# Optimization experiments

Hardware: AMD Instinct MI355X
Metric: run time of the kernel (lower is better)

Reference implementation:

```python
import jax, jax.numpy as jnp
import numpy as np

N = 256    # number of target crystals
FB = 256   # backbone output features
D = 64     # embedding_dim
H = 4      # num_heads
DH = 128   # head_dim
L = 4      # layers
BD = 128   # expansion_size == bias_dim
AK = 100   # amd_k (edge feature dim)
EPS = 1e-5


def mish(x):
    return x * jnp.tanh(jax.nn.softplus(x))


def layernorm(x, g, b):
    m = x.mean(-1, keepdims=True)
    v = x.var(-1, keepdims=True)
    return (x - m) / jnp.sqrt(v + EPS) * g + b


def setup_inputs() -> dict:
    key = jax.random.key(0)
    ks = jax.random.split(key, 16)

    def xavier(k, shape):
        fan_in, fan_out = shape[-2], shape[-1]
        lim = float(np.sqrt(6.0 / (fan_in + fan_out)))
        return jax.random.uniform(k, shape, jnp.float32, -lim, lim)

    return dict(
        target_node_features=jax.random.normal(ks[0], (N, FB), jnp.float32),
        target_edge_features=jax.random.uniform(ks[1], (N, AK), jnp.float32),
        neighbor_target=jax.random.normal(ks[2], (N, 1), jnp.float32),
        embW=xavier(ks[3], (FB, D)), embB=jnp.zeros((D,), jnp.float32),
        boutW=xavier(ks[4], (FB, 1)), boutB=jnp.zeros((1,), jnp.float32),
        qpW=xavier(ks[5], (L, D, H * DH)), qpB=jnp.zeros((L, H * DH), jnp.float32),
        kpW=xavier(ks[6], (L, D, H * DH)), kpB=jnp.zeros((L, H * DH), jnp.float32),
        qoW=xavier(ks[7], (L, H * DH, D)), qoB=jnp.zeros((L, D), jnp.float32),
        koW=xavier(ks[8], (L, H * DH, D)), koB=jnp.zeros((L, D), jnp.float32),
        bpW=xavier(ks[9], (L, BD, H * BD)), bpB=jnp.zeros((L, H * BD), jnp.float32),
        bowW=xavier(ks[10], (L, H * BD, BD)), bowB=jnp.zeros((L, BD), jnp.float32),
        qlnG=jnp.ones((L, D), jnp.float32), qlnB=jnp.zeros((L, D), jnp.float32),
        klnG=jnp.ones((L, D), jnp.float32), klnB=jnp.zeros((L, D), jnp.float32),
    )


def reference(target_node_features, target_edge_features, neighbor_target,
              embW, embB, boutW, boutB, qpW, qpB, kpW, kpB, qoW, qoB,
              koW, koB, bpW, bpB, bowW, bowB, qlnG, qlnB, klnG, klnB):
    n = target_node_features.shape[0]
    dt = target_node_features.dtype
    eye = jnp.eye(n, dtype=dt)
    # neighbors=None path: mask = [1 - I | I], shape [N, 2N]
    mask = jnp.concatenate([1.0 - eye, eye], axis=1)

    predictions = target_node_features @ boutW + boutB          # [N,1]
    node = target_node_features @ embW + embB                   # [N,D]
    q = node
    k = jnp.concatenate([node, node], axis=0)                   # [2N,D]
    edge = jnp.concatenate([target_edge_features, target_edge_features], axis=0)  # [2N,AK]

    # cdist(target_edge, edge) with safe sqrt (zero on the exact-duplicate pairs)
    diff = target_edge_features[:, None, :] - edge[None, :, :]
    sq = jnp.sum(diff * diff, axis=-1)                           # [N,2N]
    d = jnp.where(sq > 0, jnp.sqrt(jnp.where(sq > 0, sq, 1.0)), 0.0)

    # RBFExpansion(vmin=0, vmax=cutoff=1, bins=BD): gamma = 1/mean(diff(centers))
    centers = jnp.linspace(0.0, 1.0, BD).astype(dt)
    gamma = jnp.asarray(BD - 1, dt)
    bias = jnp.exp(-gamma * (d[..., None] - centers) ** 2)       # [N,2N,BD]

    v = jnp.concatenate([neighbor_target, predictions], axis=0)  # [2N,1]

    for l in range(L):
        pq = (q @ qpW[l] + qpB[l]).reshape(n, H, DH)             # [N,H,DH]
        pk = (k @ kpW[l] + kpB[l]).reshape(2 * n, H, DH)         # [2N,H,DH]
        b = jnp.einsum('nmb,bo->nmo', bias, bpW[l]) + bpB[l]     # [N,2N,H*BD]
        diffs = jnp.linalg.norm(b.reshape(n, 2 * n, H, BD), axis=-1)  # [N,2N,H]
        logits = jnp.einsum('nhd,mhd->hnm', pq, pk) / jnp.sqrt(jnp.asarray(DH, dt))
        logits = logits + diffs.transpose(2, 0, 1)               # [H,N,2N]
        logits = jnp.where(mask[None] == 0, -9e15, logits)
        attn = jax.nn.softmax(logits, axis=-1)
        vals = jnp.einsum('hnm,mo->hno', attn, v)                # [H,N,1]
        predictions = jnp.mean(vals[:, :, 0].T, axis=-1, keepdims=True)  # [N,1]
        # permute(1,2,0).reshape: layout is (head_dim, head) interleave
        pq_flat = pq.transpose(0, 2, 1).reshape(n, H * DH)
        pk_flat = pk.transpose(0, 2, 1).reshape(2 * n, H * DH)
        q = layernorm(q + mish(pq_flat @ qoW[l] + qoB[l]), qlnG[l], qlnB[l])
        k = layernorm(k + mish(pk_flat @ koW[l] + koB[l]), klnG[l], klnB[l])
        bias = mish(jnp.einsum('nmb,bo->nmo', b, bowW[l]) + bowB[l])   # [N,2N,BD]
        v = jnp.concatenate([neighbor_target, predictions], axis=0)

    return predictions
```

## Files before the change

kernel.cpp:

```cpp
#include <hip/hip_runtime.h>

struct Params {
  const float *X, *E, *nbr;
  const float *embW, *embB, *boutW, *boutB;
  const float *qpW, *qpB, *kpW, *kpB, *qoW, *qoB, *koW, *koB;
  const float *bpW, *bpB, *bowW, *bowB;
  const float *qlnG, *qlnB, *klnG, *klnB;
  float *out;
  float *pkT;
  float *clsDiff;
  unsigned *bar;
};

__device__ __forceinline__ float mishf(float x) {
  float sp = (x > 20.f) ? x : log1pf(expf(x));
  return x * tanhf(sp);
}

__device__ __forceinline__ void fma4(float4& acc, float s, const float4& v) {
  acc.x = fmaf(s, v.x, acc.x);
  acc.y = fmaf(s, v.y, acc.y);
  acc.z = fmaf(s, v.z, acc.z);
  acc.w = fmaf(s, v.w, acc.w);
}

#define LOAD8(Wp_, J0_, STRIDE_) \
  const float4 w0 = (Wp_)[(size_t)((J0_) + 0) * (STRIDE_)]; \
  const float4 w1 = (Wp_)[(size_t)((J0_) + 1) * (STRIDE_)]; \
  const float4 w2 = (Wp_)[(size_t)((J0_) + 2) * (STRIDE_)]; \
  const float4 w3 = (Wp_)[(size_t)((J0_) + 3) * (STRIDE_)]; \
  const float4 w4 = (Wp_)[(size_t)((J0_) + 4) * (STRIDE_)]; \
  const float4 w5 = (Wp_)[(size_t)((J0_) + 5) * (STRIDE_)]; \
  const float4 w6 = (Wp_)[(size_t)((J0_) + 6) * (STRIDE_)]; \
  const float4 w7 = (Wp_)[(size_t)((J0_) + 7) * (STRIDE_)];

__device__ __forceinline__ void gridBarrier(unsigned* bar, unsigned nblocks) {
  __syncthreads();
  if (threadIdx.x == 0) {
    __threadfence();
    unsigned old = atomicAdd(bar, 1u);
    if (old == nblocks - 1u) {
      atomicExch(bar + 16, 1u);
    } else {
      while (atomicAdd(bar + 16, 0u) == 0u) {
        __builtin_amdgcn_s_sleep(2);
      }
    }
    __threadfence();
  }
  __syncthreads();
}

__device__ void rare_pipe(float* row, float* drow,
                          const float* __restrict__ Wp, const float* __restrict__ Bp,
                          const float* __restrict__ Wo, const float* __restrict__ Bo,
                          float* smW, float* smS, int t) {
  const int lane = t & 63, wave = t >> 6;
  __syncthreads();
  { const int o = t & 511, kh = t >> 9;
    const float* Wc = Wp + (kh * 64) * 512 + o;
    const float* rc = row + kh * 64;
    float a = (kh == 0) ? Bp[o] : 0.f;
    #pragma unroll 8
    for (int c = 0; c < 64; ++c) a = fmaf(rc[c], Wc[c * 512], a);
    smW[t] = a; }
  __syncthreads();
  if (t < 512) smS[t] = smW[t] + smW[512 + t];
  __syncthreads();
  if (wave < 4) {
    float e1 = smS[wave * 128 + lane], e2 = smS[wave * 128 + 64 + lane];
    float s = e1 * e1 + e2 * e2;
    #pragma unroll
    for (int sh = 32; sh; sh >>= 1) s += __shfl_xor(s, sh);
    if (lane == 0) drow[wave] = sqrtf(s);
  }
  { const int c = t & 127, ch = t >> 7;
    const float* Woc = Wo + (ch * 64) * 128 + c;
    const float* bc = smS + ch * 64;
    float a = 0.f;
    #pragma unroll 8
    for (int o2 = 0; o2 < 64; ++o2) a = fmaf(bc[o2], Woc[o2 * 128], a);
    smW[t] = a; }
  __syncthreads();
  if (t < 128) {
    float a = Bo[t];
    #pragma unroll
    for (int j = 0; j < 8; ++j) a += smW[t + 128 * j];
    row[t] = mishf(a);
  }
  __syncthreads();
}

__global__ void __launch_bounds__(1024)
__attribute__((amdgpu_waves_per_eu(4, 4)))
crakn(Params P) {
  const int b = blockIdx.x, t = threadIdx.x;
  const int lane = t & 63, wave = t >> 6;
  const int nA = 2 * b, nB = 2 * b + 1;

  __shared__ __align__(16) float smPQA[2048];
  __shared__ __align__(16) float smPQB[2048];
  __shared__ __align__(16) float smKrA[512], smKrB[512];
  __shared__ __align__(16) float smQA[64], smQB[64], smKqA[64], smKqB[64];
  __shared__ __align__(16) float smNbr[256];
  __shared__ int   smMapA[256], smMapB[256];
  __shared__ float smDiff[32];
  __shared__ __align__(16) float smPDA[4096], smPDB[4096];
  __shared__ __align__(16) float rowBuf[512];
  __shared__ float smPredA, smPredB;
  __shared__ int   smIA[257], smIB[257];
  __shared__ float smDA[256], smDB[256];
  __shared__ __align__(16) float4 smP4A[1024];
  __shared__ __align__(16) float4 smP4B[1024];
  __shared__ __align__(16) float smW[1024], smB2[1024], smX2[1024], smY2[1024];
  __shared__ float smH[128];

  if (b == 128) {
    if (t < 128) {
      float c = (float)t * (1.f / 127.f);
      rowBuf[t] = expf(-127.f * c * c);
      rowBuf[128 + t] = 0.f;
    }
    __syncthreads();
    for (int l = 0; l < 4; ++l) {
      const float* rowCur = rowBuf + (l & 1) * 256;
      float* rowNxt = rowBuf + ((l + 1) & 1) * 256;
      { const int o4 = t & 127, kc = t >> 7;
        const float4* Wf = (const float4*)(P.bpW + (size_t)l * 65536) + (size_t)(kc * 16) * 128 + o4;
        float4 az = {0.f,0.f,0.f,0.f}, ag = {0.f,0.f,0.f,0.f};
        { LOAD8(Wf, 0, 128);
          const int r = kc * 16;
          fma4(az, rowCur[r+0], w0); fma4(ag, rowCur[128+r+0], w0);
          fma4(az, rowCur[r+1], w1); fma4(ag, rowCur[128+r+1], w1);
          fma4(az, rowCur[r+2], w2); fma4(ag, rowCur[128+r+2], w2);
          fma4(az, rowCur[r+3], w3); fma4(ag, rowCur[128+r+3], w3);
          fma4(az, rowCur[r+4], w4); fma4(ag, rowCur[128+r+4], w4);
          fma4(az, rowCur[r+5], w5); fma4(ag, rowCur[128+r+5], w5);
          fma4(az, rowCur[r+6], w6); fma4(ag, rowCur[128+r+6], w6);
          fma4(az, rowCur[r+7], w7); fma4(ag, rowCur[128+r+7], w7);
        }
        { LOAD8(Wf, 8, 128);
          const int r = kc * 16 + 8;
          fma4(az, rowCur[r+0], w0); fma4(ag, rowCur[128+r+0], w0);
          fma4(az, rowCur[r+1], w1); fma4(ag, rowCur[128+r+1], w1);
          fma4(az, rowCur[r+2], w2); fma4(ag, rowCur[128+r+2], w2);
          fma4(az, rowCur[r+3], w3); fma4(ag, rowCur[128+r+3], w3);
          fma4(az, rowCur[r+4], w4); fma4(ag, rowCur[128+r+4], w4);
          fma4(az, rowCur[r+5], w5); fma4(ag, rowCur[128+r+5], w5);
          fma4(az, rowCur[r+6], w6); fma4(ag, rowCur[128+r+6], w6);
          fma4(az, rowCur[r+7], w7); fma4(ag, rowCur[128+r+7], w7);
        }
        smP4A[t] = az; smP4B[t] = ag; }
      __syncthreads();
      if (t < 512) {
        const float* pa = (const float*)smP4A;
        const float* pb = (const float*)smP4B;
        float bp = P.bpB[l * 512 + t];
        float z = bp, g2 = bp;
        #pragma unroll
        for (int kc = 0; kc < 8; ++kc) { z += pa[kc * 512 + t]; g2 += pb[kc * 512 + t]; }
        smW[t] = z; smB2[t] = g2;
      }
      __syncthreads();
      if (wave < 8) {
        const int cls = wave >> 2, h = wave & 3;
        const float* arr = cls ? smB2 : smW;
        float e1 = arr[h * 128 + lane], e2 = arr[h * 128 + 64 + lane];
        float s = e1 * e1 + e2 * e2;
        #pragma unroll
        for (int sh = 32; sh; sh >>= 1) s += __shfl_xor(s, sh);
        if (lane == 0) P.clsDiff[(l * 2 + cls) * 4 + h] = sqrtf(s);
      }
      if (l < 3) {
        { const int o4 = t & 31, kc = t >> 5;
          const float4* Wf = (const float4*)(P.bowW + (size_t)l * 65536) + (size_t)(kc * 16) * 32 + o4;
          float4 az = {0.f,0.f,0.f,0.f}, ag = {0.f,0.f,0.f,0.f};
          { LOAD8(Wf, 0, 32);
            const int r = kc * 16;
            fma4(az, smW[r+0], w0); fma4(ag, smB2[r+0], w0);
            fma4(az, smW[r+1], w1); fma4(ag, smB2[r+1], w1);
            fma4(az, smW[r+2], w2); fma4(ag, smB2[r+2], w2);
            fma4(az, smW[r+3], w3); fma4(ag, smB2[r+3], w3);
            fma4(az, smW[r+4], w4); fma4(ag, smB2[r+4], w4);
            fma4(az, smW[r+5], w5); fma4(ag, smB2[r+5], w5);
            fma4(az, smW[r+6], w6); fma4(ag, smB2[r+6], w6);
            fma4(az, smW[r+7], w7); fma4(ag, smB2[r+7], w7);
          }
          { LOAD8(Wf, 8, 32);
            const int r = kc * 16 + 8;
            fma4(az, smW[r+0], w0); fma4(ag, smB2[r+0], w0);
            fma4(az, smW[r+1], w1); fma4(ag, smB2[r+1], w1);
            fma4(az, smW[r+2], w2); fma4(ag, smB2[r+2], w2);
            fma4(az, smW[r+3], w3); fma4(ag, smB2[r+3], w3);
            fma4(az, smW[r+4], w4); fma4(ag, smB2[r+4], w4);
            fma4(az, smW[r+5], w5); fma4(ag, smB2[r+5], w5);
            fma4(az, smW[r+6], w6); fma4(ag, smB2[r+6], w6);
            fma4(az, smW[r+7], w7); fma4(ag, smB2[r+7], w7);
          }
          smP4A[t] = az; smP4B[t] = ag; }
        __syncthreads();
        if (t < 128) {
          const float* pa = (const float*)smP4A;
          const float* pb = (const float*)smP4B;
          float bo = P.bowB[l * 128 + t];
          float sz = 0.f, sg = 0.f;
          #pragma unroll
          for (int kc = 0; kc < 32; ++kc) { sz += pa[kc * 128 + t]; sg += pb[kc * 128 + t]; }
          rowNxt[t] = mishf(sz + bo);
          rowNxt[128 + t] = mishf(sg + bo);
        }
        __syncthreads();
      }
    }
  } else {
    if (t < 256) {
      smX2[t] = P.X[(size_t)nA * 256 + t];
      smY2[t] = P.X[(size_t)nB * 256 + t];
      smNbr[t] = P.nbr[t];
    }
    if (t == 0) { smIA[256] = 0; smIB[256] = 0; }
    __syncthreads();
    { const int d = t & 63, ch = t >> 6;
      const float* W = P.embW + (ch * 16) * 64 + d;
      const float* xrA = smX2 + ch * 16;
      const float* xrB = smY2 + ch * 16;
      float aA = 0.f, aB = 0.f;
      #pragma unroll
      for (int f = 0; f < 16; ++f) {
        float w = W[f * 64];
        aA = fmaf(xrA[f], w, aA);
        aB = fmaf(xrB[f], w, aB);
      }
      smW[t] = aA; smB2[t] = aB; }
    { float pp = 0.f;
      if (t < 256) pp = smX2[t] * P.boutW[t];
      else if (t < 512) pp = smY2[t - 256] * P.boutW[t - 256];
      #pragma unroll
      for (int s = 32; s; s >>= 1) pp += __shfl_xor(pp, s);
      if (t < 512 && lane == 0) smH[wave] = pp; }
    __syncthreads();
    if (t < 64) {
      float ndA = P.embB[t], ndB = P.embB[t];
      #pragma unroll
      for (int j = 0; j < 16; ++j) { ndA += smW[t + 64 * j]; ndB += smB2[t + 64 * j]; }
      smQA[t] = ndA; smKqA[t] = ndA;
      smQB[t] = ndB; smKqB[t] = ndB;
    }
    if (t == 0) {
      smPredA = smH[0] + smH[1] + smH[2] + smH[3] + P.boutB[0];
      smPredB = smH[4] + smH[5] + smH[6] + smH[7] + P.boutB[0];
    }
    if (t < 25) {
      ((float4*)rowBuf)[t]         = ((const float4*)(P.E + (size_t)nA * 100))[t];
      ((float4*)(rowBuf + 128))[t] = ((const float4*)(P.E + (size_t)nB * 100))[t];
    }
    __syncthreads();
    if (t < 512) {
      const int m = t & 255, cr = t >> 8;
      const float4* em = (const float4*)(P.E + (size_t)m * 100);
      const float4* en = (const float4*)(cr ? (rowBuf + 128) : rowBuf);
      float sq = 0.f;
      #pragma unroll 5
      for (int jj = 0; jj < 25; ++jj) {
        float4 a = en[jj], c = em[jj];
        float dx = a.x - c.x, dy = a.y - c.y, dz = a.z - c.z, dw = a.w - c.w;
        sq += dx * dx + dy * dy + dz * dz + dw * dw;
      }
      float dd = (sq > 0.f) ? sqrtf(sq) : 0.f;
      int mv;
      if (dd == 0.f) mv = -2;
      else if (dd < 1.905f) {
        int* sI = cr ? smIB : smIA;
        float* sD = cr ? smDB : smDA;
        int i = atomicAdd(&sI[256], 1);
        sI[i] = m; sD[i] = dd;
        mv = i;
      } else mv = -1;
      (cr ? smMapB : smMapA)[m] = mv;
    }
    __syncthreads();
    { int cntA = smIA[256]; if (cntA > 256) cntA = 256;
      int cntB = smIB[256]; if (cntB > 256) cntB = 256;
      if (cntA + cntB > 0) {
        for (int i = 0; i < cntA; ++i) {
          if (t < 128) {
            float dd = smDA[i] - (float)t * (1.f / 127.f);
            smY2[t] = expf(-127.f * dd * dd);
          }
          for (int l = 0; l < 4; ++l)
            rare_pipe(smY2, smPDA + i * 16 + l * 4,
                      P.bpW + (size_t)l * 65536, P.bpB + l * 512,
                      P.bowW + (size_t)l * 65536, P.bowB + l * 128, smW, smX2, t);
        }
        for (int i = 0; i < cntB; ++i) {
          if (t < 128) {
            float dd = smDB[i] - (float)t * (1.f / 127.f);
            smY2[t] = expf(-127.f * dd * dd);
          }
          for (int l = 0; l < 4; ++l)
            rare_pipe(smY2, smPDB + i * 16 + l * 4,
                      P.bpW + (size_t)l * 65536, P.bpB + l * 512,
                      P.bowW + (size_t)l * 65536, P.bowB + l * 128, smW, smX2, t);
        }
      } }
    __syncthreads();

    for (int l = 0; l < 4; ++l) {
      { const int g = t >> 9, u = t & 511;
        const int o4 = u & 127, kc = u >> 7;
        const float4* Wf = (const float4*)((g ? P.kpW : P.qpW) + (size_t)l * 32768)
                         + (size_t)(kc * 16) * 128 + o4;
        const float* xa = g ? smKqA : smQA;
        const float* xb = g ? smKqB : smQB;
        float4 aA = {0.f,0.f,0.f,0.f}, aB = {0.f,0.f,0.f,0.f};
        { LOAD8(Wf, 0, 128);
          const int r = kc * 16;
          fma4(aA, xa[r+0], w0); fma4(aB, xb[r+0], w0);
          fma4(aA, xa[r+1], w1); fma4(aB, xb[r+1], w1);
          fma4(aA, xa[r+2], w2); fma4(aB, xb[r+2], w2);
          fma4(aA, xa[r+3], w3); fma4(aB, xb[r+3], w3);
          fma4(aA, xa[r+4], w4); fma4(aB, xb[r+4], w4);
          fma4(aA, xa[r+5], w5); fma4(aB, xb[r+5], w5);
          fma4(aA, xa[r+6], w6); fma4(aB, xb[r+6], w6);
          fma4(aA, xa[r+7], w7); fma4(aB, xb[r+7], w7);
        }
        { LOAD8(Wf, 8, 128);
          const int r = kc * 16 + 8;
          fma4(aA, xa[r+0], w0); fma4(aB, xb[r+0], w0);
          fma4(aA, xa[r+1], w1); fma4(aB, xb[r+1], w1);
          fma4(aA, xa[r+2], w2); fma4(aB, xb[r+2], w2);
          fma4(aA, xa[r+3], w3); fma4(aB, xb[r+3], w3);
          fma4(aA, xa[r+4], w4); fma4(aB, xb[r+4], w4);
          fma4(aA, xa[r+5], w5); fma4(aB, xb[r+5], w5);
          fma4(aA, xa[r+6], w6); fma4(aB, xb[r+6], w6);
          fma4(aA, xa[r+7], w7); fma4(aB, xb[r+7], w7);
        }
        smP4A[t] = aA; smP4B[t] = aB; }
      __syncthreads();
      { const int g = t >> 9, o = t & 511;
        const float* pa = (const float*)smP4A + g * 2048;
        const float* pb = (const float*)smP4B + g * 2048;
        float b0 = (g ? P.kpB : P.qpB)[l * 512 + o];
        float vA = b0 + pa[o] + pa[512 + o] + pa[1024 + o] + pa[1536 + o];
        float vB = b0 + pb[o] + pb[512 + o] + pb[1024 + o] + pb[1536 + o];
        if (g) {
          smKrA[o] = vA; smKrB[o] = vB;
          float2 st; st.x = vA; st.y = vB;
          *(float2*)(P.pkT + (size_t)l * 131072 + (size_t)o * 256 + nA) = st;
        } else { smPQA[l * 512 + o] = vA; smPQB[l * 512 + o] = vB; } }
      __syncthreads();
      if (l < 3) {
        { const int g = t >> 9, u = t & 511;
          const int o4 = u & 15, kc = u >> 4;
          const float4* Wf = (const float4*)((g ? P.koW : P.qoW) + (size_t)l * 32768)
                           + (size_t)(kc * 16) * 16 + o4;
          const float* prA = g ? smKrA : (smPQA + l * 512);
          const float* prB = g ? smKrB : (smPQB + l * 512);
          const int pb0 = kc * 4;
          float4 aA = {0.f,0.f,0.f,0.f}, aB = {0.f,0.f,0.f,0.f};
          { LOAD8(Wf, 0, 16);
            fma4(aA, prA[pb0 + 0],       w0); fma4(aB, prB[pb0 + 0],       w0);
            fma4(aA, prA[128 + pb0],     w1); fma4(aB, prB[128 + pb0],     w1);
            fma4(aA, prA[256 + pb0],     w2); fma4(aB, prB[256 + pb0],     w2);
            fma4(aA, prA[384 + pb0],     w3); fma4(aB, prB[384 + pb0],     w3);
            fma4(aA, prA[pb0 + 1],       w4); fma4(aB, prB[pb0 + 1],       w4);
            fma4(aA, prA[128 + pb0 + 1], w5); fma4(aB, prB[128 + pb0 + 1], w5);
            fma4(aA, prA[256 + pb0 + 1], w6); fma4(aB, prB[256 + pb0 + 1], w6);
            fma4(aA, prA[384 + pb0 + 1], w7); fma4(aB, prB[384 + pb0 + 1], w7);
          }
          { LOAD8(Wf, 8, 16);
            fma4(aA, prA[pb0 + 2],       w0); fma4(aB, prB[pb0 + 2],       w0);
            fma4(aA, prA[128 + pb0 + 2], w1); fma4(aB, prB[128 + pb0 + 2], w1);
            fma4(aA, prA[256 + pb0 + 2], w2); fma4(aB, prB[256 + pb0 + 2], w2);
            fma4(aA, prA[384 + pb0 + 2], w3); fma4(aB, prB[384 + pb0 + 2], w3);
            fma4(aA, prA[pb0 + 3],       w4); fma4(aB, prB[pb0 + 3],       w4);
            fma4(aA, prA[128 + pb0 + 3], w5); fma4(aB, prB[128 + pb0 + 3], w5);
            fma4(aA, prA[256 + pb0 + 3], w6); fma4(aB, prB[256 + pb0 + 3], w6);
            fma4(aA, prA[384 + pb0 + 3], w7); fma4(aB, prB[384 + pb0 + 3], w7);
          }
          smP4A[t] = aA; smP4B[t] = aB; }
        __syncthreads();
        { const int g = t >> 9, u = t & 511;
          if (u < 128) {
            const int cr = u >> 6, uu = u & 63;
            const float* src = (const float*)(cr ? smP4B : smP4A) + g * 2048;
            float acc = (g ? P.koB : P.qoB)[l * 64 + uu];
            #pragma unroll
            for (int kc = 0; kc < 32; ++kc) acc += src[kc * 64 + uu];
            float* x = g ? (cr ? smKqB : smKqA) : (cr ? smQB : smQA);
            float xv = x[uu] + mishf(acc);
            float mean = xv;
            #pragma unroll
            for (int s = 32; s; s >>= 1) mean += __shfl_xor(mean, s);
            mean *= (1.f / 64.f);
            float dv = xv - mean, var = dv * dv;
            #pragma unroll
            for (int s = 32; s; s >>= 1) var += __shfl_xor(var, s);
            var *= (1.f / 64.f);
            const float* G  = (g ? P.klnG : P.qlnG) + l * 64;
            const float* Bb = (g ? P.klnB : P.qlnB) + l * 64;
            x[uu] = dv * rsqrtf(var + 1e-5f) * G[uu] + Bb[uu];
          } }
        __syncthreads();
      }
    }
  }

  gridBarrier(P.bar, 129);
  if (b >= 128) return;

  if (t < 32) smDiff[t] = P.clsDiff[t];
  __syncthreads();
  {
    const int l = t >> 8, h = (t >> 6) & 3, mq = lane;
    const float* qvA = smPQA + l * 512 + h * 128;
    const float* qvB = smPQB + l * 512 + h * 128;
    const float4* pt4 = (const float4*)P.pkT + (size_t)l * 32768 + (size_t)h * 128 * 64 + mq;
    float4 dA = {0.f, 0.f, 0.f, 0.f}, dB = {0.f, 0.f, 0.f, 0.f};
    for (int jb = 0; jb < 16; ++jb) {
      const int j0 = jb * 8;
      LOAD8(pt4, j0, 64);
      fma4(dA, qvA[j0+0], w0); fma4(dB, qvB[j0+0], w0);
      fma4(dA, qvA[j0+1], w1); fma4(dB, qvB[j0+1], w1);
      fma4(dA, qvA[j0+2], w2); fma4(dB, qvB[j0+2], w2);
      fma4(dA, qvA[j0+3], w3); fma4(dB, qvB[j0+3], w3);
      fma4(dA, qvA[j0+4], w4); fma4(dB, qvB[j0+4], w4);
      fma4(dA, qvA[j0+5], w5); fma4(dB, qvB[j0+5], w5);
      fma4(dA, qvA[j0+6], w6); fma4(dB, qvB[j0+6], w6);
      fma4(dA, qvA[j0+7], w7); fma4(dB, qvB[j0+7], w7);
    }
    auto epi = [&](const float4& dot, const int* sMap, const float* sPD, int nn, float* oH) {
      float dArr[4] = {dot.x, dot.y, dot.z, dot.w};
      float lg[4], nb[4];
      int self = -1;
      #pragma unroll
      for (int i = 0; i < 4; ++i) {
        const int m = mq * 4 + i;
        const int cls = sMap[m];
        const float bd = (cls == -2) ? smDiff[(l * 2 + 0) * 4 + h]
                       : (cls == -1) ? smDiff[(l * 2 + 1) * 4 + h]
                       : sPD[cls * 16 + l * 4 + h];
        lg[i] = dArr[i] * 0.08838834764831845f + bd;
        nb[i] = smNbr[m];
        if (m == nn) { self = i; nb[i] = 0.f; }
      }
      float wm = fmaxf(fmaxf(lg[0], lg[1]), fmaxf(lg[2], lg[3]));
      #pragma unroll
      for (int s = 32; s; s >>= 1) wm = fmaxf(wm, __shfl_xor(wm, s));
      float sA = 0.f, sB = 0.f, sD = 0.f;
      #pragma unroll
      for (int i = 0; i < 4; ++i) {
        float e = expf(lg[i] - wm);
        sD += e;
        sA = fmaf(e, nb[i], sA);
        if (i == self) sB = e;
      }
      #pragma unroll
      for (int s = 32; s; s >>= 1) {
        sA += __shfl_xor(sA, s); sB += __shfl_xor(sB, s); sD += __shfl_xor(sD, s);
      }
      if (lane == 0) { oH[wave] = sA; oH[16 + wave] = sB; oH[32 + wave] = sD; }
    };
    epi(dA, smMapA, smPDA, nA, smH);
    epi(dB, smMapB, smPDB, nB, smH + 48);
  }
  __syncthreads();
  if (t == 0 || t == 64) {
    const float* H = (t == 0) ? smH : smH + 48;
    float p = (t == 0) ? smPredA : smPredB;
    #pragma unroll
    for (int l = 0; l < 4; ++l) {
      float np = 0.f;
      #pragma unroll
      for (int h = 0; h < 4; ++h) {
        const int w = l * 4 + h;
        np += 0.25f * ((H[w] + H[16 + w] * p) / H[32 + w]);
      }
      p = np;
    }
    P.out[(t == 0) ? nA : nB] = p;
  }
}

extern "C" void kernel_launch(void* const* d_in, const int* in_sizes, int n_in,
                              void* d_out, int out_size, void* d_ws, size_t ws_size,
                              hipStream_t stream) {
  char* p = (char*)d_ws;
  auto carve = [&](size_t bytes) -> void* {
    void* r = (void*)p;
    p += (bytes + 255) & ~(size_t)255;
    return r;
  };

  Params P;
  P.X     = (const float*)d_in[0];
  P.E     = (const float*)d_in[1];
  P.nbr   = (const float*)d_in[2];
  P.embW  = (const float*)d_in[3];
  P.embB  = (const float*)d_in[4];
  P.boutW = (const float*)d_in[5];
  P.boutB = (const float*)d_in[6];
  P.qpW   = (const float*)d_in[7];
  P.qpB   = (const float*)d_in[8];
  P.kpW   = (const float*)d_in[9];
  P.kpB   = (const float*)d_in[10];
  P.qoW   = (const float*)d_in[11];
  P.qoB   = (const float*)d_in[12];
  P.koW   = (const float*)d_in[13];
  P.koB   = (const float*)d_in[14];
  P.bpW   = (const float*)d_in[15];
  P.bpB   = (const float*)d_in[16];
  P.bowW  = (const float*)d_in[17];
  P.bowB  = (const float*)d_in[18];
  P.qlnG  = (const float*)d_in[19];
  P.qlnB  = (const float*)d_in[20];
  P.klnG  = (const float*)d_in[21];
  P.klnB  = (const float*)d_in[22];
  P.out   = (float*)d_out;

  P.pkT     = (float*)carve((size_t)4 * 512 * 256 * 4);
  P.clsDiff = (float*)carve((size_t)32 * 4);
  P.bar     = (unsigned*)carve(256);

  hipMemsetAsync(P.bar, 0, 256, stream);

  hipLaunchKernelGGL(crakn, dim3(129), dim3(1024), 0, stream, P);
}
```

Before: 162.8 us.

## Process four crystals per block to halve grid size and reuse weight loads

```diff
diff --git a/kernel.cpp b/kernel.cpp
--- a/kernel.cpp
+++ b/kernel.cpp
@@ -91,31 +91,27 @@
   __syncthreads();
 }
 
-__global__ void __launch_bounds__(1024)
-__attribute__((amdgpu_waves_per_eu(4, 4)))
-crakn(Params P) {
+__global__ void __launch_bounds__(1024, 4) crakn(Params P) {
   const int b = blockIdx.x, t = threadIdx.x;
   const int lane = t & 63, wave = t >> 6;
-  const int nA = 2 * b, nB = 2 * b + 1;
-
-  __shared__ __align__(16) float smPQA[2048];
-  __shared__ __align__(16) float smPQB[2048];
-  __shared__ __align__(16) float smKrA[512], smKrB[512];
-  __shared__ __align__(16) float smQA[64], smQB[64], smKqA[64], smKqB[64];
+
+  __shared__ __align__(16) float smPQA[2048], smPQB[2048], smPQC[2048], smPQD[2048];
+  __shared__ __align__(16) float smKrA[512], smKrB[512], smKrC[512], smKrD[512];
+  __shared__ __align__(16) float smQA[64], smQB[64], smQC[64], smQD[64];
+  __shared__ __align__(16) float smKqA[64], smKqB[64], smKqC[64], smKqD[64];
   __shared__ __align__(16) float smNbr[256];
-  __shared__ int   smMapA[256], smMapB[256];
+  __shared__ int   smMap4[1024];
   __shared__ float smDiff[32];
-  __shared__ __align__(16) float smPDA[4096], smPDB[4096];
+  __shared__ __align__(16) float smPD4[4096];
   __shared__ __align__(16) float rowBuf[512];
-  __shared__ float smPredA, smPredB;
-  __shared__ int   smIA[257], smIB[257];
-  __shared__ float smDA[256], smDB[256];
-  __shared__ __align__(16) float4 smP4A[1024];
-  __shared__ __align__(16) float4 smP4B[1024];
+  __shared__ float smPred4[4];
+  __shared__ int   smI4[1028];
+  __shared__ float smD4[1024];
+  __shared__ __align__(16) float4 smP4A[1024], smP4B[1024];
   __shared__ __align__(16) float smW[1024], smB2[1024], smX2[1024], smY2[1024];
-  __shared__ float smH[128];
-
-  if (b == 128) {
+  __shared__ float smH[192];
+
+  if (b == 64) {
     if (t < 128) {
       float c = (float)t * (1.f / 127.f);
       rowBuf[t] = expf(-127.f * c * c);
@@ -213,52 +209,53 @@
       }
     }
   } else {
-    if (t < 256) {
-      smX2[t] = P.X[(size_t)nA * 256 + t];
-      smY2[t] = P.X[(size_t)nB * 256 + t];
-      smNbr[t] = P.nbr[t];
-    }
-    if (t == 0) { smIA[256] = 0; smIB[256] = 0; }
+    float* xS = (float*)smP4A;
+    if (t < 256) smNbr[t] = P.nbr[t];
+    xS[t] = P.X[(size_t)(4 * b + (t >> 8)) * 256 + (t & 255)];
+    if (t < 4) smI4[t * 257 + 256] = 0;
     __syncthreads();
     { const int d = t & 63, ch = t >> 6;
       const float* W = P.embW + (ch * 16) * 64 + d;
-      const float* xrA = smX2 + ch * 16;
-      const float* xrB = smY2 + ch * 16;
-      float aA = 0.f, aB = 0.f;
+      float aA = 0.f, aB = 0.f, aC = 0.f, aD = 0.f;
       #pragma unroll
       for (int f = 0; f < 16; ++f) {
         float w = W[f * 64];
-        aA = fmaf(xrA[f], w, aA);
-        aB = fmaf(xrB[f], w, aB);
-      }
-      smW[t] = aA; smB2[t] = aB; }
-    { float pp = 0.f;
-      if (t < 256) pp = smX2[t] * P.boutW[t];
-      else if (t < 512) pp = smY2[t - 256] * P.boutW[t - 256];
+        const int x0 = ch * 16 + f;
+        aA = fmaf(xS[x0],       w, aA);
+        aB = fmaf(xS[256 + x0], w, aB);
+        aC = fmaf(xS[512 + x0], w, aC);
+        aD = fmaf(xS[768 + x0], w, aD);
+      }
+      smW[t] = aA; smB2[t] = aB; smX2[t] = aC; smY2[t] = aD; }
+    { float pp = xS[t] * P.boutW[t & 255];
       #pragma unroll
       for (int s = 32; s; s >>= 1) pp += __shfl_xor(pp, s);
-      if (t < 512 && lane == 0) smH[wave] = pp; }
+      if (lane == 0) smH[wave] = pp; }
     __syncthreads();
     if (t < 64) {
-      float ndA = P.embB[t], ndB = P.embB[t];
-      #pragma unroll
-      for (int j = 0; j < 16; ++j) { ndA += smW[t + 64 * j]; ndB += smB2[t + 64 * j]; }
-      smQA[t] = ndA; smKqA[t] = ndA;
-      smQB[t] = ndB; smKqB[t] = ndB;
+      float ndA = P.embB[t], ndB = ndA, ndC = ndA, ndD = ndA;
+      #pragma unroll
+      for (int j = 0; j < 16; ++j) {
+        ndA += smW[t + 64 * j]; ndB += smB2[t + 64 * j];
+        ndC += smX2[t + 64 * j]; ndD += smY2[t + 64 * j];
+      }
+      smQA[t] = ndA; smKqA[t] = ndA;  smQB[t] = ndB; smKqB[t] = ndB;
+      smQC[t] = ndC; smKqC[t] = ndC;  smQD[t] = ndD; smKqD[t] = ndD;
     }
     if (t == 0) {
-      smPredA = smH[0] + smH[1] + smH[2] + smH[3] + P.boutB[0];
-      smPredB = smH[4] + smH[5] + smH[6] + smH[7] + P.boutB[0];
-    }
-    if (t < 25) {
-      ((float4*)rowBuf)[t]         = ((const float4*)(P.E + (size_t)nA * 100))[t];
-      ((float4*)(rowBuf + 128))[t] = ((const float4*)(P.E + (size_t)nB * 100))[t];
+      #pragma unroll
+      for (int cr = 0; cr < 4; ++cr)
+        smPred4[cr] = smH[cr*4] + smH[cr*4+1] + smH[cr*4+2] + smH[cr*4+3] + P.boutB[0];
+    }
+    if (t < 128) {
+      const int cr = t >> 5, j = t & 31;
+      if (j < 25)
+        ((float4*)rowBuf)[cr * 32 + j] = ((const float4*)(P.E + (size_t)(4 * b + cr) * 100))[j];
     }
     __syncthreads();
-    if (t < 512) {
-      const int m = t & 255, cr = t >> 8;
+    { const int m = t & 255, cr = t >> 8;
       const float4* em = (const float4*)(P.E + (size_t)m * 100);
-      const float4* en = (const float4*)(cr ? (rowBuf + 128) : rowBuf);
+      const float4* en = (const float4*)(rowBuf + cr * 128);
       float sq = 0.f;
       #pragma unroll 5
       for (int jj = 0; jj < 25; ++jj) {
@@ -270,144 +267,161 @@
       int mv;
       if (dd == 0.f) mv = -2;
       else if (dd < 1.905f) {
-        int* sI = cr ? smIB : smIA;
-        float* sD = cr ? smDB : smDA;
-        int i = atomicAdd(&sI[256], 1);
-        sI[i] = m; sD[i] = dd;
-        mv = i;
+        int i = atomicAdd(&smI4[cr * 257 + 256], 1);
+        if (i < 256) { smI4[cr * 257 + i] = m; smD4[cr * 256 + i] = dd; }
+        mv = (i < 64) ? i : -1;
       } else mv = -1;
-      (cr ? smMapB : smMapA)[m] = mv;
+      smMap4[cr * 256 + m] = mv;
     }
     __syncthreads();
-    { int cntA = smIA[256]; if (cntA > 256) cntA = 256;
-      int cntB = smIB[256]; if (cntB > 256) cntB = 256;
-      if (cntA + cntB > 0) {
-        for (int i = 0; i < cntA; ++i) {
-          if (t < 128) {
-            float dd = smDA[i] - (float)t * (1.f / 127.f);
-            smY2[t] = expf(-127.f * dd * dd);
-          }
-          for (int l = 0; l < 4; ++l)
-            rare_pipe(smY2, smPDA + i * 16 + l * 4,
-                      P.bpW + (size_t)l * 65536, P.bpB + l * 512,
-                      P.bowW + (size_t)l * 65536, P.bowB + l * 128, smW, smX2, t);
-        }
-        for (int i = 0; i < cntB; ++i) {
-          if (t < 128) {
-            float dd = smDB[i] - (float)t * (1.f / 127.f);
-            smY2[t] = expf(-127.f * dd * dd);
-          }
-          for (int l = 0; l < 4; ++l)
-            rare_pipe(smY2, smPDB + i * 16 + l * 4,
-                      P.bpW + (size_t)l * 65536, P.bpB + l * 512,
-                      P.bowW + (size_t)l * 65536, P.bowB + l * 128, smW, smX2, t);
-        }
-      } }
+    for (int cr = 0; cr < 4; ++cr) {
+      int cnt = smI4[cr * 257 + 256]; if (cnt > 64) cnt = 64;
+      for (int i = 0; i < cnt; ++i) {
+        if (t < 128) {
+          float dd = smD4[cr * 256 + i] - (float)t * (1.f / 127.f);
+          smY2[t] = expf(-127.f * dd * dd);
+        }
+        for (int l = 0; l < 4; ++l)
+          rare_pipe(smY2, smPD4 + (cr * 64 + i) * 16 + l * 4,
+                    P.bpW + (size_t)l * 65536, P.bpB + l * 512,
+                    P.bowW + (size_t)l * 65536, P.bowB + l * 128, smW, smX2, t);
+      }
+    }
     __syncthreads();
 
     for (int l = 0; l < 4; ++l) {
+      float4 aA = {0.f,0.f,0.f,0.f}, aB = {0.f,0.f,0.f,0.f};
+      float4 aC = {0.f,0.f,0.f,0.f}, aD = {0.f,0.f,0.f,0.f};
       { const int g = t >> 9, u = t & 511;
         const int o4 = u & 127, kc = u >> 7;
         const float4* Wf = (const float4*)((g ? P.kpW : P.qpW) + (size_t)l * 32768)
                          + (size_t)(kc * 16) * 128 + o4;
         const float* xa = g ? smKqA : smQA;
         const float* xb = g ? smKqB : smQB;
-        float4 aA = {0.f,0.f,0.f,0.f}, aB = {0.f,0.f,0.f,0.f};
+        const float* xc = g ? smKqC : smQC;
+        const float* xd = g ? smKqD : smQD;
         { LOAD8(Wf, 0, 128);
           const int r = kc * 16;
-          fma4(aA, xa[r+0], w0); fma4(aB, xb[r+0], w0);
-          fma4(aA, xa[r+1], w1); fma4(aB, xb[r+1], w1);
-          fma4(aA, xa[r+2], w2); fma4(aB, xb[r+2], w2);
-          fma4(aA, xa[r+3], w3); fma4(aB, xb[r+3], w3);
-          fma4(aA, xa[r+4], w4); fma4(aB, xb[r+4], w4);
-          fma4(aA, xa[r+5], w5); fma4(aB, xb[r+5], w5);
-          fma4(aA, xa[r+6], w6); fma4(aB, xb[r+6], w6);
-          fma4(aA, xa[r+7], w7); fma4(aB, xb[r+7], w7);
+          fma4(aA, xa[r+0], w0); fma4(aB, xb[r+0], w0); fma4(aC, xc[r+0], w0); fma4(aD, xd[r+0], w0);
+          fma4(aA, xa[r+1], w1); fma4(aB, xb[r+1], w1); fma4(aC, xc[r+1], w1); fma4(aD, xd[r+1], w1);
+          fma4(aA, xa[r+2], w2); fma4(aB, xb[r+2], w2); fma4(aC, xc[r+2], w2); fma4(aD, xd[r+2], w2);
+          fma4(aA, xa[r+3], w3); fma4(aB, xb[r+3], w3); fma4(aC, xc[r+3], w3); fma4(aD, xd[r+3], w3);
+          fma4(aA, xa[r+4], w4); fma4(aB, xb[r+4], w4); fma4(aC, xc[r+4], w4); fma4(aD, xd[r+4], w4);
+          fma4(aA, xa[r+5], w5); fma4(aB, xb[r+5], w5); fma4(aC, xc[r+5], w5); fma4(aD, xd[r+5], w5);
+          fma4(aA, xa[r+6], w6); fma4(aB, xb[r+6], w6); fma4(aC, xc[r+6], w6); fma4(aD, xd[r+6], w6);
+          fma4(aA, xa[r+7], w7); fma4(aB, xb[r+7], w7); fma4(aC, xc[r+7], w7); fma4(aD, xd[r+7], w7);
         }
         { LOAD8(Wf, 8, 128);
           const int r = kc * 16 + 8;
-          fma4(aA, xa[r+0], w0); fma4(aB, xb[r+0], w0);
-          fma4(aA, xa[r+1], w1); fma4(aB, xb[r+1], w1);
-          fma4(aA, xa[r+2], w2); fma4(aB, xb[r+2], w2);
-          fma4(aA, xa[r+3], w3); fma4(aB, xb[r+3], w3);
-          fma4(aA, xa[r+4], w4); fma4(aB, xb[r+4], w4);
-          fma4(aA, xa[r+5], w5); fma4(aB, xb[r+5], w5);
-          fma4(aA, xa[r+6], w6); fma4(aB, xb[r+6], w6);
-          fma4(aA, xa[r+7], w7); fma4(aB, xb[r+7], w7);
-        }
-        smP4A[t] = aA; smP4B[t] = aB; }
+          fma4(aA, xa[r+0], w0); fma4(aB, xb[r+0], w0); fma4(aC, xc[r+0], w0); fma4(aD, xd[r+0], w0);
+          fma4(aA, xa[r+1], w1); fma4(aB, xb[r+1], w1); fma4(aC, xc[r+1], w1); fma4(aD, xd[r+1], w1);
+          fma4(aA, xa[r+2], w2); fma4(aB, xb[r+2], w2); fma4(aC, xc[r+2], w2); fma4(aD, xd[r+2], w2);
+          fma4(aA, xa[r+3], w3); fma4(aB, xb[r+3], w3); fma4(aC, xc[r+3], w3); fma4(aD, xd[r+3], w3);
+          fma4(aA, xa[r+4], w4); fma4(aB, xb[r+4], w4); fma4(aC, xc[r+4], w4); fma4(aD, xd[r+4], w4);
+          fma4(aA, xa[r+5], w5); fma4(aB, xb[r+5], w5); fma4(aC, xc[r+5], w5); fma4(aD, xd[r+5], w5);
+          fma4(aA, xa[r+6], w6); fma4(aB, xb[r+6], w6); fma4(aC, xc[r+6], w6); fma4(aD, xd[r+6], w6);
+          fma4(aA, xa[r+7], w7); fma4(aB, xb[r+7], w7); fma4(aC, xc[r+7], w7); fma4(aD, xd[r+7], w7);
+        }
+      }
+      smP4A[t] = aA; smP4B[t] = aB;
+      __syncthreads();
+      float vA, vB;
+      { const int g = t >> 9, o = t & 511;
+        const float* pa = (const float*)smP4A + g * 2048;
+        const float* pb = (const float*)smP4B + g * 2048;
+        float b0 = (g ? P.kpB : P.qpB)[l * 512 + o];
+        vA = b0 + pa[o] + pa[512 + o] + pa[1024 + o] + pa[1536 + o];
+        vB = b0 + pb[o] + pb[512 + o] + pb[1024 + o] + pb[1536 + o]; }
+      __syncthreads();
+      smP4A[t] = aC; smP4B[t] = aD;
       __syncthreads();
       { const int g = t >> 9, o = t & 511;
         const float* pa = (const float*)smP4A + g * 2048;
         const float* pb = (const float*)smP4B + g * 2048;
         float b0 = (g ? P.kpB : P.qpB)[l * 512 + o];
-        float vA = b0 + pa[o] + pa[512 + o] + pa[1024 + o] + pa[1536 + o];
-        float vB = b0 + pb[o] + pb[512 + o] + pb[1024 + o] + pb[1536 + o];
+        float vC = b0 + pa[o] + pa[512 + o] + pa[1024 + o] + pa[1536 + o];
+        float vD = b0 + pb[o] + pb[512 + o] + pb[1024 + o] + pb[1536 + o];
         if (g) {
-          smKrA[o] = vA; smKrB[o] = vB;
-          float2 st; st.x = vA; st.y = vB;
-          *(float2*)(P.pkT + (size_t)l * 131072 + (size_t)o * 256 + nA) = st;
-        } else { smPQA[l * 512 + o] = vA; smPQB[l * 512 + o] = vB; } }
+          smKrA[o] = vA; smKrB[o] = vB; smKrC[o] = vC; smKrD[o] = vD;
+          float4 st; st.x = vA; st.y = vB; st.z = vC; st.w = vD;
+          *(float4*)(P.pkT + (size_t)l * 131072 + (size_t)o * 256 + 4 * b) = st;
+        } else {
+          smPQA[l * 512 + o] = vA; smPQB[l * 512 + o] = vB;
+          smPQC[l * 512 + o] = vC; smPQD[l * 512 + o] = vD;
+        } }
       __syncthreads();
       if (l < 3) {
+        float4 cA = {0.f,0.f,0.f,0.f}, cB = {0.f,0.f,0.f,0.f};
+        float4 cC = {0.f,0.f,0.f,0.f}, cD = {0.f,0.f,0.f,0.f};
         { const int g = t >> 9, u = t & 511;
           const int o4 = u & 15, kc = u >> 4;
           const float4* Wf = (const float4*)((g ? P.koW : P.qoW) + (size_t)l * 32768)
                            + (size_t)(kc * 16) * 16 + o4;
-          const float* prA = g ? smKrA : (smPQA + l * 512);
-          const float* prB = g ? smKrB : (smPQB + l * 512);
-          const int pb0 = kc * 4;
-          float4 aA = {0.f,0.f,0.f,0.f}, aB = {0.f,0.f,0.f,0.f};
+          const float* pA = g ? smKrA : (smPQA + l * 512);
+          const float* pB = g ? smKrB : (smPQB + l * 512);
+          const float* pC = g ? smKrC : (smPQC + l * 512);
+          const float* pD = g ? smKrD : (smPQD + l * 512);
+          const int p0 = kc * 4;
           { LOAD8(Wf, 0, 16);
-            fma4(aA, prA[pb0 + 0],       w0); fma4(aB, prB[pb0 + 0],       w0);
-            fma4(aA, prA[128 + pb0],     w1); fma4(aB, prB[128 + pb0],     w1);
-            fma4(aA, prA[256 + pb0],     w2); fma4(aB, prB[256 + pb0],     w2);
-            fma4(aA, prA[384 + pb0],     w3); fma4(aB, prB[384 + pb0],     w3);
-            fma4(aA, prA[pb0 + 1],       w4); fma4(aB, prB[pb0 + 1],       w4);
-            fma4(aA, prA[128 + pb0 + 1], w5); fma4(aB, prB[128 + pb0 + 1], w5);
-            fma4(aA, prA[256 + pb0 + 1], w6); fma4(aB, prB[256 + pb0 + 1], w6);
-            fma4(aA, prA[384 + pb0 + 1], w7); fma4(aB, prB[384 + pb0 + 1], w7);
+            fma4(cA, pA[p0+0],     w0); fma4(cB, pB[p0+0],     w0); fma4(cC, pC[p0+0],     w0); fma4(cD, pD[p0+0],     w0);
+            fma4(cA, pA[128+p0],   w1); fma4(cB, pB[128+p0],   w1); fma4(cC, pC[128+p0],   w1); fma4(cD, pD[128+p0],   w1);
+            fma4(cA, pA[256+p0],   w2); fma4(cB, pB[256+p0],   w2); fma4(cC, pC[256+p0],   w2); fma4(cD, pD[256+p0],   w2);
+            fma4(cA, pA[384+p0],   w3); fma4(cB, pB[384+p0],   w3); fma4(cC, pC[384+p0],   w3); fma4(cD, pD[384+p0],   w3);
+            fma4(cA, pA[p0+1],     w4); fma4(cB, pB[p0+1],     w4); fma4(cC, pC[p0+1],     w4); fma4(cD, pD[p0+1],     w4);
+            fma4(cA, pA[128+p0+1], w5); fma4(cB, pB[128+p0+1], w5); fma4(cC, pC[128+p0+1], w5); fma4(cD, pD[128+p0+1], w5);
+            fma4(cA, pA[256+p0+1], w6); fma4(cB, pB[256+p0+1], w6); fma4(cC, pC[256+p0+1], w6); fma4(cD, pD[256+p0+1], w6);
+            fma4(cA, pA[384+p0+1], w7); fma4(cB, pB[384+p0+1], w7); fma4(cC, pC[384+p0+1], w7); fma4(cD, pD[384+p0+1], w7);
           }
           { LOAD8(Wf, 8, 16);
-            fma4(aA, prA[pb0 + 2],       w0); fma4(aB, prB[pb0 + 2],       w0);
-            fma4(aA, prA[128 + pb0 + 2], w1); fma4(aB, prB[128 + pb0 + 2], w1);
-            fma4(aA, prA[256 + pb0 + 2], w2); fma4(aB, prB[256 + pb0 + 2], w2);
-            fma4(aA, prA[384 + pb0 + 2], w3); fma4(aB, prB[384 + pb0 + 2], w3);
-            fma4(aA, prA[pb0 + 3],       w4); fma4(aB, prB[pb0 + 3],       w4);
-            fma4(aA, prA[128 + pb0 + 3], w5); fma4(aB, prB[128 + pb0 + 3], w5);
-            fma4(aA, prA[256 + pb0 + 3], w6); fma4(aB, prB[256 + pb0 + 3], w6);
-            fma4(aA, prA[384 + pb0 + 3], w7); fma4(aB, prB[384 + pb0 + 3], w7);
+            fma4(cA, pA[p0+2],     w0); fma4(cB, pB[p0+2],     w0); fma4(cC, pC[p0+2],     w0); fma4(cD, pD[p0+2],     w0);
+            fma4(cA, pA[128+p0+2], w1); fma4(cB, pB[128+p0+2], w1); fma4(cC, pC[128+p0+2], w1); fma4(cD, pD[128+p0+2], w1);
+            fma4(cA, pA[256+p0+2], w2); fma4(cB, pB[256+p0+2], w2); fma4(cC, pC[256+p0+2], w2); fma4(cD, pD[256+p0+2], w2);
+            fma4(cA, pA[384+p0+2], w3); fma4(cB, pB[384+p0+2], w3); fma4(cC, pC[384+p0+2], w3); fma4(cD, pD[384+p0+2], w3);
+            fma4(cA, pA[p0+3],     w4); fma4(cB, pB[p0+3],     w4); fma4(cC, pC[p0+3],     w4); fma4(cD, pD[p0+3],     w4);
+            fma4(cA, pA[128+p0+3], w5); fma4(cB, pB[128+p0+3], w5); fma4(cC, pC[128+p0+3], w5); fma4(cD, pD[128+p0+3], w5);
+            fma4(cA, pA[256+p0+3], w6); fma4(cB, pB[256+p0+3], w6); fma4(cC, pC[256+p0+3], w6); fma4(cD, pD[256+p0+3], w6);
+            fma4(cA, pA[384+p0+3], w7); fma4(cB, pB[384+p0+3], w7); fma4(cC, pC[384+p0+3], w7); fma4(cD, pD[384+p0+3], w7);
           }
-          smP4A[t] = aA; smP4B[t] = aB; }
+        }
+        smP4A[t] = cA; smP4B[t] = cB;
         __syncthreads();
-        { const int g = t >> 9, u = t & 511;
-          if (u < 128) {
-            const int cr = u >> 6, uu = u & 63;
-            const float* src = (const float*)(cr ? smP4B : smP4A) + g * 2048;
-            float acc = (g ? P.koB : P.qoB)[l * 64 + uu];
-            #pragma unroll
-            for (int kc = 0; kc < 32; ++kc) acc += src[kc * 64 + uu];
-            float* x = g ? (cr ? smKqB : smKqA) : (cr ? smQB : smQA);
-            float xv = x[uu] + mishf(acc);
-            float mean = xv;
-            #pragma unroll
-            for (int s = 32; s; s >>= 1) mean += __shfl_xor(mean, s);
-            mean *= (1.f / 64.f);
-            float dv = xv - mean, var = dv * dv;
-            #pragma unroll
-            for (int s = 32; s; s >>= 1) var += __shfl_xor(var, s);
-            var *= (1.f / 64.f);
-            const float* G  = (g ? P.klnG : P.qlnG) + l * 64;
-            const float* Bb = (g ? P.klnB : P.qlnB) + l * 64;
-            x[uu] = dv * rsqrtf(var + 1e-5f) * G[uu] + Bb[uu];
-          } }
-        __syncthreads();
+        #pragma unroll
+        for (int pass = 0; pass < 2; ++pass) {
+          { const int g = t >> 9, u = t & 511;
+            if (u < 128) {
+              const int cr2 = u >> 6, uu = u & 63;
+              const float* src = (const float*)(cr2 ? smP4B : smP4A) + g * 2048;
+              float acc = (g ? P.koB : P.qoB)[l * 64 + uu];
+              #pragma unroll
+              for (int kc = 0; kc < 32; ++kc) acc += src[kc * 64 + uu];
+              float* x;
+              if (pass == 0) x = g ? (cr2 ? smKqB : smKqA) : (cr2 ? smQB : smQA);
+              else           x = g ? (cr2 ? smKqD : smKqC) : (cr2 ? smQD : smQC);
+              float xv = x[uu] + mishf(acc);
+              float mean = xv;
+              #pragma unroll
+              for (int s = 32; s; s >>= 1) mean += __shfl_xor(mean, s);
+              mean *= (1.f / 64.f);
+              float dv = xv - mean, var = dv * dv;
+              #pragma unroll
+              for (int s = 32; s; s >>= 1) var += __shfl_xor(var, s);
+              var *= (1.f / 64.f);
+              const float* G  = (g ? P.klnG : P.qlnG) + l * 64;
+              const float* Bb = (g ? P.klnB : P.qlnB) + l * 64;
+              x[uu] = dv * rsqrtf(var + 1e-5f) * G[uu] + Bb[uu];
+            } }
+          __syncthreads();
+          if (pass == 0) {
+            smP4A[t] = cC; smP4B[t] = cD;
+            __syncthreads();
+          }
+        }
       }
     }
   }
 
-  gridBarrier(P.bar, 129);
-  if (b >= 128) return;
+  gridBarrier(P.bar, 65);
+  if (b >= 64) return;
 
   if (t < 32) smDiff[t] = P.clsDiff[t];
   __syncthreads();
@@ -415,19 +429,22 @@
     const int l = t >> 8, h = (t >> 6) & 3, mq = lane;
     const float* qvA = smPQA + l * 512 + h * 128;
     const float* qvB = smPQB + l * 512 + h * 128;
+    const float* qvC = smPQC + l * 512 + h * 128;
+    const float* qvD = smPQD + l * 512 + h * 128;
     const float4* pt4 = (const float4*)P.pkT + (size_t)l * 32768 + (size_t)h * 128 * 64 + mq;
-    float4 dA = {0.f, 0.f, 0.f, 0.f}, dB = {0.f, 0.f, 0.f, 0.f};
+    float4 dA = {0.f,0.f,0.f,0.f}, dB = {0.f,0.f,0.f,0.f};
+    float4 dC = {0.f,0.f,0.f,0.f}, dD = {0.f,0.f,0.f,0.f};
     for (int jb = 0; jb < 16; ++jb) {
       const int j0 = jb * 8;
       LOAD8(pt4, j0, 64);
-      fma4(dA, qvA[j0+0], w0); fma4(dB, qvB[j0+0], w0);
-      fma4(dA, qvA[j0+1], w1); fma4(dB, qvB[j0+1], w1);
-      fma4(dA, qvA[j0+2], w2); fma4(dB, qvB[j0+2], w2);
-      fma4(dA, qvA[j0+3], w3); fma4(dB, qvB[j0+3], w3);
-      fma4(dA, qvA[j0+4], w4); fma4(dB, qvB[j0+4], w4);
-      fma4(dA, qvA[j0+5], w5); fma4(dB, qvB[j0+5], w5);
-      fma4(dA, qvA[j0+6], w6); fma4(dB, qvB[j0+6], w6);
-      fma4(dA, qvA[j0+7], w7); fma4(dB, qvB[j0+7], w7);
+      fma4(dA, qvA[j0+0], w0); fma4(dB, qvB[j0+0], w0); fma4(dC, qvC[j0+0], w0); fma4(dD, qvD[j0+0], w0);
+      fma4(dA, qvA[j0+1], w1); fma4(dB, qvB[j0+1], w1); fma4(dC, qvC[j0+1], w1); fma4(dD, qvD[j0+1], w1);
+      fma4(dA, qvA[j0+2], w2); fma4(dB, qvB[j0+2], w2); fma4(dC, qvC[j0+2], w2); fma4(dD, qvD[j0+2], w2);
+      fma4(dA, qvA[j0+3], w3); fma4(dB, qvB[j0+3], w3); fma4(dC, qvC[j0+3], w3); fma4(dD, qvD[j0+3], w3);
+      fma4(dA, qvA[j0+4], w4); fma4(dB, qvB[j0+4], w4); fma4(dC, qvC[j0+4], w4); fma4(dD, qvD[j0+4], w4);
+      fma4(dA, qvA[j0+5], w5); fma4(dB, qvB[j0+5], w5); fma4(dC, qvC[j0+5], w5); fma4(dD, qvD[j0+5], w5);
+      fma4(dA, qvA[j0+6], w6); fma4(dB, qvB[j0+6], w6); fma4(dC, qvC[j0+6], w6); fma4(dD, qvD[j0+6], w6);
+      fma4(dA, qvA[j0+7], w7); fma4(dB, qvB[j0+7], w7); fma4(dC, qvC[j0+7], w7); fma4(dD, qvD[j0+7], w7);
     }
     auto epi = [&](const float4& dot, const int* sMap, const float* sPD, int nn, float* oH) {
       float dArr[4] = {dot.x, dot.y, dot.z, dot.w};
@@ -461,13 +478,16 @@
       }
       if (lane == 0) { oH[wave] = sA; oH[16 + wave] = sB; oH[32 + wave] = sD; }
     };
-    epi(dA, smMapA, smPDA, nA, smH);
-    epi(dB, smMapB, smPDB, nB, smH + 48);
+    epi(dA, smMap4,       smPD4,        4 * b + 0, smH);
+    epi(dB, smMap4 + 256, smPD4 + 1024, 4 * b + 1, smH + 48);
+    epi(dC, smMap4 + 512, smPD4 + 2048, 4 * b + 2, smH + 96);
+    epi(dD, smMap4 + 768, smPD4 + 3072, 4 * b + 3, smH + 144);
   }
   __syncthreads();
-  if (t == 0 || t == 64) {
-    const float* H = (t == 0) ? smH : smH + 48;
-    float p = (t == 0) ? smPredA : smPredB;
+  if (t == 0 || t == 64 || t == 128 || t == 192) {
+    const int cr = t >> 6;
+    const float* H = smH + cr * 48;
+    float p = smPred4[cr];
     #pragma unroll
     for (int l = 0; l < 4; ++l) {
       float np = 0.f;
@@ -478,7 +498,7 @@
       }
       p = np;
     }
-    P.out[(t == 0) ? nA : nB] = p;
+    P.out[4 * b + cr] = p;
   }
 }
 
@@ -524,5 +544,5 @@
 
   hipMemsetAsync(P.bar, 0, 256, stream);
 
-  hipLaunchKernelGGL(crakn, dim3(129), dim3(1024), 0, stream, P);
+  hipLaunchKernelGGL(crakn, dim3(65), dim3(1024), 0, stream, P);
 }
```

Measured after the change: 195.0 us. 19.8% more time.
